# Optimization experiments

Measured on AMD Instinct MI355X. Metric: run time of the kernel, lower is better.

Reference implementation:

```python
import jax, jax.numpy as jnp
import numpy as np

B, IN, H, NOPT = 16384, 4096, 128, 64
GAIN = 0.5  # default control_gains value in the module


def gru_cell(x, h, Wih, Whh, bih, bhh):
    # torch GRU single step; gate order r, z, n
    gi = x @ Wih + bih          # [B, 3H]
    gh = h @ Whh + bhh          # [B, 3H]
    ir, iz, inn = jnp.split(gi, 3, axis=-1)
    hr, hz, hn = jnp.split(gh, 3, axis=-1)
    r = jax.nn.sigmoid(ir + hr)
    z = jax.nn.sigmoid(iz + hz)
    n = jnp.tanh(inn + r * hn)
    return (1.0 - z) * n + z * h


def setup_inputs() -> dict:
    key = jax.random.key(0)
    ks = jax.random.split(key, 12)
    s = lambda k, shape: (jax.random.normal(k, shape, jnp.float32) * 0.05)
    return {
        "obs": jax.random.normal(ks[0], (B, IN), jnp.float32),
        "chosen_option": jax.random.randint(ks[1], (B,), 0, NOPT),
        "h0": jnp.zeros((B, H), jnp.float32),
        "h1": jnp.zeros((B, H), jnp.float32),
        "Wa": s(ks[2], (IN, H)), "ba": jnp.zeros((H,), jnp.float32),
        "Wih0": s(ks[3], (H, 3 * H)), "Whh0": s(ks[4], (H, 3 * H)),
        "bih0": jnp.zeros((3 * H,), jnp.float32), "bhh0": jnp.zeros((3 * H,), jnp.float32),
        "Wih1": s(ks[5], (2 * H, 3 * H)), "Whh1": s(ks[6], (H, 3 * H)),
        "bih1": jnp.zeros((3 * H,), jnp.float32), "bhh1": jnp.zeros((3 * H,), jnp.float32),
        "Wv0": s(ks[7], (H, NOPT)), "bv0": jnp.zeros((NOPT,), jnp.float32),
        "Wv1": s(ks[8], (H, NOPT)), "bv1": jnp.zeros((NOPT,), jnp.float32),
        "Wt0": s(ks[9], (H, NOPT)), "bt0": jnp.zeros((NOPT,), jnp.float32),
    }


def reference(obs, chosen_option, h0, h1, Wa, ba, Wih0, Whh0, bih0, bhh0,
              Wih1, Whh1, bih1, bhh1, Wv0, bv0, Wv1, bv1, Wt0, bt0):
    # attention: tanh(Linear(obs))
    attn = jnp.tanh(obs @ Wa + ba)                       # [B, H]
    # layer 0: GRU on attn
    h0n = gru_cell(attn, h0, Wih0, Whh0, bih0, bhh0)     # [B, H]
    hc0 = (h0n - 0.5) * GAIN + 0.5                       # gain contrast
    v0 = hc0 @ Wv0 + bv0                                 # [B, NOPT]
    term = jax.nn.sigmoid(hc0 @ Wt0 + bt0)               # [B, NOPT]
    term_p = jnp.take_along_axis(term, chosen_option[:, None], axis=1)  # [B, 1]
    # layer 1: GRU on cat(attn, own hidden)
    x1 = jnp.concatenate([attn, h1], axis=-1)            # [B, 2H]
    h1n = gru_cell(x1, h1, Wih1, Whh1, bih1, bhh1)       # [B, H]
    hc1 = (h1n - 0.5) * GAIN + 0.5
    v1 = hc1 @ Wv1 + bv1                                 # [B, NOPT]
    return v0, term_p, v1, h0n, h1n
```

## Files before the change

kernel.cpp:

```cpp
#include <hip/hip_runtime.h>
#include <hip/hip_bf16.h>
#include <stdint.h>


typedef __attribute__((ext_vector_type(8))) short bf16x8;
typedef __attribute__((ext_vector_type(4))) float f32x4;
typedef __attribute__((ext_vector_type(8))) float f32x8;

#define INDIM 4096
#define H 128
#define NOPT 64

#define WS_WAT    0u
#define WS_WIH0T  524288u
#define WS_WHH0T  573440u
#define WS_WIH1T  622592u
#define WS_WHH1T  720896u
#define WS_WV0T   770048u
#define WS_WV1T   778240u
#define WS_WT0T   786432u
#define WS_ATTN   794624u

#define OUT_V0    0u
#define OUT_TERMP 1048576u
#define OUT_V1    1064960u
#define OUT_H0N   2113536u
#define OUT_H1N   4210688u

typedef __attribute__((address_space(1))) const void gas_t;
typedef __attribute__((address_space(3))) void las_t;
static __device__ __forceinline__ void gll16(const void* g, void* l) {
  __builtin_amdgcn_global_load_lds((gas_t*)g, (las_t*)l, 16, 0, 0);
}

static __device__ __forceinline__ uint16_t f2bf(float f) {
  __hip_bfloat16 h = __float2bfloat16(f);
  return __builtin_bit_cast(uint16_t, h);
}
static __device__ __forceinline__ float sigm(float x) { return 1.0f / (1.0f + __expf(-x)); }
static __device__ __forceinline__ float fast_tanh(float x) {
  float e = __expf(2.0f * x);
  return 1.0f - 2.0f / (e + 1.0f);
}
static __device__ __forceinline__ f32x4 mfma16(bf16x8 a, bf16x8 b, f32x4 c) {
  return __builtin_amdgcn_mfma_f32_16x16x32_bf16(a, b, c, 0, 0, 0);
}
static __device__ __forceinline__ bf16x8 cvt8(f32x8 v) {
  bf16x8 r;
#pragma unroll
  for (int j = 0; j < 8; ++j) r[j] = (short)f2bf(v[j]);
  return r;
}

__global__ void k_transpose(const float* __restrict__ Wa,
                            const float* __restrict__ Wih0,
                            const float* __restrict__ Whh0,
                            const float* __restrict__ Wih1,
                            const float* __restrict__ Whh1,
                            const float* __restrict__ Wv0,
                            const float* __restrict__ Wv1,
                            const float* __restrict__ Wt0,
                            uint16_t* __restrict__ ws) {
  __shared__ float sT[32][34];
  int blk = blockIdx.x;
  const float* in; uint16_t* out; int K; int N; int base;
  if (blk < 512)      { in = Wa;   out = ws + WS_WAT;   K = 4096; N = 128; base = 0; }
  else if (blk < 560) { in = Wih0; out = ws + WS_WIH0T; K = 128;  N = 384; base = 512; }
  else if (blk < 608) { in = Whh0; out = ws + WS_WHH0T; K = 128;  N = 384; base = 560; }
  else if (blk < 704) { in = Wih1; out = ws + WS_WIH1T; K = 256;  N = 384; base = 608; }
  else if (blk < 752) { in = Whh1; out = ws + WS_WHH1T; K = 128;  N = 384; base = 704; }
  else if (blk < 760) { in = Wv0;  out = ws + WS_WV0T;  K = 128;  N = 64;  base = 752; }
  else if (blk < 768) { in = Wv1;  out = ws + WS_WV1T;  K = 128;  N = 64;  base = 760; }
  else                { in = Wt0;  out = ws + WS_WT0T;  K = 128;  N = 64;  base = 768; }
  const int tix = blk - base;
  const int nTK = K >> 5;
  const int kt = tix & (nTK - 1);
  const int nt = tix / nTK;
  const int k0 = kt * 32, n0 = nt * 32;
  const int t = threadIdx.x;
#pragma unroll
  for (int i = 0; i < 4; ++i) {
    int e = i * 256 + t, kk = e >> 5, nn = e & 31;
    sT[kk][nn] = in[(size_t)(k0 + kk) * N + n0 + nn];
  }
  __syncthreads();
#pragma unroll
  for (int i = 0; i < 4; ++i) {
    int e = i * 256 + t, nn = e >> 5, kk = e & 31;
    out[(size_t)(n0 + nn) * K + k0 + kk] = f2bf(sT[kk][nn]);
  }
}

__launch_bounds__(256, 2)
__global__ void k_attn(const float* __restrict__ obs,
                       uint16_t* __restrict__ ws,
                       const float* __restrict__ ba) {
  __shared__ __align__(16) uint16_t sA[2][32 * 8 * 8];
  __shared__ __align__(16) uint16_t sB[2][128 * 8 * 8];
  const uint16_t* WaT = ws + WS_WAT;
  uint16_t* attn = ws + WS_ATTN;
  const int t = threadIdx.x, w = t >> 6, lane = t & 63;
  const int l15 = lane & 15, quad = lane >> 4;
  const int wm = w >> 1, wn = w & 1;
  const int row0 = blockIdx.x * 32;
  const int rA = wm * 16 + l15;
  const int sr = t >> 3, sg = t & 7;
  const float* aSrc = obs + (size_t)(row0 + sr) * INDIM + sg * 8;
  const int aDst = (sr * 8 + (sg ^ (sr & 7))) * 8;
  const int n0 = w * 32 + (lane >> 3);
  const int gsrc = (lane & 7) ^ (n0 & 7);
  const uint16_t* bSrc = WaT + (size_t)n0 * INDIM + gsrc * 8;

  f32x4 acc[4] = {};

  auto compute = [&](int buf) {
#pragma unroll
    for (int ks = 0; ks < 2; ++ks) {
      bf16x8 a = *(const bf16x8*)&sA[buf][(rA * 8 + ((ks * 4 + quad) ^ (rA & 7))) * 8];
#pragma unroll
      for (int nb = 0; nb < 4; ++nb) {
        const int n = wn * 64 + nb * 16 + l15;
        bf16x8 b = *(const bf16x8*)&sB[buf][(n * 8 + ((ks * 4 + quad) ^ (n & 7))) * 8];
        acc[nb] = mfma16(a, b, acc[nb]);
      }
    }
  };

  {
    f32x8 av = *(const f32x8*)aSrc;
#pragma unroll
    for (int j = 0; j < 4; ++j)
      gll16(bSrc + (size_t)j * 8 * INDIM, (void*)&sB[0][(w * 4 + j) * 512]);
    *(bf16x8*)&sA[0][aDst] = cvt8(av);
  }
  __syncthreads();

  for (int kt = 0; kt < 63; ++kt) {
    const int cur = kt & 1, nxt = cur ^ 1;
    f32x8 av = *(const f32x8*)(aSrc + (size_t)(kt + 1) * 64);
#pragma unroll
    for (int j = 0; j < 4; ++j)
      gll16(bSrc + (size_t)(kt + 1) * 64 + (size_t)j * 8 * INDIM,
            (void*)&sB[nxt][(w * 4 + j) * 512]);
    compute(cur);
    *(bf16x8*)&sA[nxt][aDst] = cvt8(av);
    __syncthreads();
  }
  compute(1);

#pragma unroll
  for (int nb = 0; nb < 4; ++nb) {
    const int col = wn * 64 + nb * 16 + l15;
    const float bav = ba[col];
#pragma unroll
    for (int i = 0; i < 4; ++i) {
      const int r = wm * 16 + quad * 4 + i;
      attn[(size_t)(row0 + r) * H + col] = f2bf(fast_tanh(acc[nb][i] + bav));
    }
  }
}

__launch_bounds__(256, 2)
__global__ void k_gru(const uint16_t* __restrict__ ws,
                      const float* __restrict__ h0,
                      const float* __restrict__ bih0,
                      const float* __restrict__ bhh0,
                      const float* __restrict__ bv0,
                      const float* __restrict__ bt0,
                      const int* __restrict__ chosen,
                      const float* __restrict__ h1,
                      const float* __restrict__ bih1,
                      const float* __restrict__ bhh1,
                      const float* __restrict__ bv1,
                      float* __restrict__ out) {
  __shared__ __align__(16) uint16_t sC[32 * 16 * 8];
  const uint16_t* attn  = ws + WS_ATTN;
  const uint16_t* Wih0T = ws + WS_WIH0T;
  const uint16_t* Whh0T = ws + WS_WHH0T;
  const uint16_t* Wih1T = ws + WS_WIH1T;
  const uint16_t* Whh1T = ws + WS_WHH1T;
  const uint16_t* Wv0T  = ws + WS_WV0T;
  const uint16_t* Wv1T  = ws + WS_WV1T;
  const uint16_t* Wt0T  = ws + WS_WT0T;
  const int t = threadIdx.x, w = t >> 6, lane = t & 63;
  const int l15 = lane & 15, quad = lane >> 4;
  const int wm = w >> 1, wn = w & 1;
  const int row0 = blockIdx.x * 32;
  const int rA = wm * 16 + l15;

  bf16x8 ax[4], ah[4];
#pragma unroll
  for (int ks = 0; ks < 4; ++ks) {
    ax[ks] = *(const bf16x8*)(attn + (size_t)(row0 + rA) * H + ks * 32 + quad * 8);
    ah[ks] = cvt8(*(const f32x8*)(h0 + (size_t)(row0 + rA) * H + ks * 32 + quad * 8));
  }

#pragma unroll
  for (int nbl = 0; nbl < 4; ++nbl) {
    const int nb = wn * 4 + nbl;
    const int nrow = nb * 16 + l15;
    f32x4 air = {}, ahr = {}, aiz = {}, ahz = {}, ain = {}, ahn = {};
#pragma unroll
    for (int ks = 0; ks < 4; ++ks) {
      const int k = ks * 32 + quad * 8;
      bf16x8 b0 = *(const bf16x8*)(Wih0T + (size_t)(nrow      ) * H + k);
      bf16x8 b1 = *(const bf16x8*)(Wih0T + (size_t)(nrow + 128) * H + k);
      bf16x8 b2 = *(const bf16x8*)(Wih0T + (size_t)(nrow + 256) * H + k);
      bf16x8 b3 = *(const bf16x8*)(Whh0T + (size_t)(nrow      ) * H + k);
      bf16x8 b4 = *(const bf16x8*)(Whh0T + (size_t)(nrow + 128) * H + k);
      bf16x8 b5 = *(const bf16x8*)(Whh0T + (size_t)(nrow + 256) * H + k);
      air = mfma16(ax[ks], b0, air);
      aiz = mfma16(ax[ks], b1, aiz);
      ain = mfma16(ax[ks], b2, ain);
      ahr = mfma16(ah[ks], b3, ahr);
      ahz = mfma16(ah[ks], b4, ahz);
      ahn = mfma16(ah[ks], b5, ahn);
    }
    const int col = nrow;
    const float b_ir = bih0[col],       b_hr = bhh0[col];
    const float b_iz = bih0[col + 128], b_hz = bhh0[col + 128];
    const float b_in = bih0[col + 256], b_hn = bhh0[col + 256];
    const int kb = col >> 3;
#pragma unroll
    for (int i = 0; i < 4; ++i) {
      const int r = wm * 16 + quad * 4 + i;
      const int grow = row0 + r;
      const float rr = sigm(air[i] + ahr[i] + b_ir + b_hr);
      const float zz = sigm(aiz[i] + ahz[i] + b_iz + b_hz);
      const float nn = fast_tanh(ain[i] + b_in + rr * (ahn[i] + b_hn));
      const float hv = h0[(size_t)grow * H + col];
      const float hnew = (1.0f - zz) * nn + zz * hv;
      out[OUT_H0N + (size_t)grow * H + col] = hnew;
      sC[(r * 16 + (kb ^ (r & 7))) * 8 + (col & 7)] = f2bf(0.5f * hnew + 0.25f);
    }
  }
  __syncthreads();

  {
    bf16x8 ac[4];
#pragma unroll
    for (int ks = 0; ks < 4; ++ks)
      ac[ks] = *(const bf16x8*)&sC[(rA * 16 + ((ks * 4 + quad) ^ (rA & 7))) * 8];
    int ch[4];
#pragma unroll
    for (int i = 0; i < 4; ++i) ch[i] = chosen[row0 + wm * 16 + quad * 4 + i];
#pragma unroll
    for (int hb = 0; hb < 2; ++hb) {
      const int colf = wn * 2 + hb;
      const int nrow = colf * 16 + l15;
      f32x4 av = {}, at = {};
#pragma unroll
      for (int ks = 0; ks < 4; ++ks) {
        const int k = ks * 32 + quad * 8;
        bf16x8 b0 = *(const bf16x8*)(Wv0T + (size_t)nrow * H + k);
        bf16x8 b1 = *(const bf16x8*)(Wt0T + (size_t)nrow * H + k);
        av = mfma16(ac[ks], b0, av);
        at = mfma16(ac[ks], b1, at);
      }
      const int col = nrow;
      const float bvv = bv0[col], btv = bt0[col];
#pragma unroll
      for (int i = 0; i < 4; ++i) {
        const int grow = row0 + wm * 16 + quad * 4 + i;
        out[OUT_V0 + (size_t)grow * NOPT + col] = av[i] + bvv;
        if (ch[i] == col)
          out[OUT_TERMP + grow] = sigm(at[i] + btv);
      }
    }
  }
  __syncthreads();

  bf16x8 ah1[4];
#pragma unroll
  for (int ks = 0; ks < 4; ++ks)
    ah1[ks] = cvt8(*(const f32x8*)(h1 + (size_t)(row0 + rA) * H + ks * 32 + quad * 8));
#pragma unroll
  for (int nbl = 0; nbl < 4; ++nbl) {
    const int nb = wn * 4 + nbl;
    const int nrow = nb * 16 + l15;
    f32x4 air = {}, ahr = {}, aiz = {}, ahz = {}, ain = {}, ahn = {};
#pragma unroll
    for (int ks = 0; ks < 8; ++ks) {
      const int k = ks * 32 + quad * 8;
      const bf16x8 a = (ks < 4) ? ax[ks] : ah1[ks - 4];
      bf16x8 b0 = *(const bf16x8*)(Wih1T + (size_t)(nrow      ) * 256 + k);
      bf16x8 b1 = *(const bf16x8*)(Wih1T + (size_t)(nrow + 128) * 256 + k);
      bf16x8 b2 = *(const bf16x8*)(Wih1T + (size_t)(nrow + 256) * 256 + k);
      air = mfma16(a, b0, air);
      aiz = mfma16(a, b1, aiz);
      ain = mfma16(a, b2, ain);
    }
#pragma unroll
    for (int ks = 0; ks < 4; ++ks) {
      const int k = ks * 32 + quad * 8;
      bf16x8 b0 = *(const bf16x8*)(Whh1T + (size_t)(nrow      ) * H + k);
      bf16x8 b1 = *(const bf16x8*)(Whh1T + (size_t)(nrow + 128) * H + k);
      bf16x8 b2 = *(const bf16x8*)(Whh1T + (size_t)(nrow + 256) * H + k);
      ahr = mfma16(ah1[ks], b0, ahr);
      ahz = mfma16(ah1[ks], b1, ahz);
      ahn = mfma16(ah1[ks], b2, ahn);
    }
    const int col = nrow;
    const float b_ir = bih1[col],       b_hr = bhh1[col];
    const float b_iz = bih1[col + 128], b_hz = bhh1[col + 128];
    const float b_in = bih1[col + 256], b_hn = bhh1[col + 256];
    const int kb = col >> 3;
#pragma unroll
    for (int i = 0; i < 4; ++i) {
      const int r = wm * 16 + quad * 4 + i;
      const int grow = row0 + r;
      const float rr = sigm(air[i] + ahr[i] + b_ir + b_hr);
      const float zz = sigm(aiz[i] + ahz[i] + b_iz + b_hz);
      const float nn = fast_tanh(ain[i] + b_in + rr * (ahn[i] + b_hn));
      const float hv = h1[(size_t)grow * H + col];
      const float hnew = (1.0f - zz) * nn + zz * hv;
      out[OUT_H1N + (size_t)grow * H + col] = hnew;
      sC[(r * 16 + (kb ^ (r & 7))) * 8 + (col & 7)] = f2bf(0.5f * hnew + 0.25f);
    }
  }
  __syncthreads();

  {
    bf16x8 ac[4];
#pragma unroll
    for (int ks = 0; ks < 4; ++ks)
      ac[ks] = *(const bf16x8*)&sC[(rA * 16 + ((ks * 4 + quad) ^ (rA & 7))) * 8];
#pragma unroll
    for (int hb = 0; hb < 2; ++hb) {
      const int colf = wn * 2 + hb;
      const int nrow = colf * 16 + l15;
      f32x4 av = {};
#pragma unroll
      for (int ks = 0; ks < 4; ++ks) {
        const int k = ks * 32 + quad * 8;
        bf16x8 b = *(const bf16x8*)(Wv1T + (size_t)nrow * H + k);
        av = mfma16(ac[ks], b, av);
      }
      const int col = nrow;
      const float bvv = bv1[col];
#pragma unroll
      for (int i = 0; i < 4; ++i) {
        const int grow = row0 + wm * 16 + quad * 4 + i;
        out[OUT_V1 + (size_t)grow * NOPT + col] = av[i] + bvv;
      }
    }
  }
}

extern "C" void kernel_launch(void* const* d_in, const int* in_sizes, int n_in,
                              void* d_out, int out_size, void* d_ws, size_t ws_size,
                              hipStream_t stream) {
  (void)in_sizes; (void)n_in; (void)out_size; (void)ws_size;
  const float* obs    = (const float*)d_in[0];
  const int*   chosen = (const int*)d_in[1];
  const float* h0     = (const float*)d_in[2];
  const float* h1     = (const float*)d_in[3];
  const float* Wa     = (const float*)d_in[4];
  const float* ba     = (const float*)d_in[5];
  const float* Wih0   = (const float*)d_in[6];
  const float* Whh0   = (const float*)d_in[7];
  const float* bih0   = (const float*)d_in[8];
  const float* bhh0   = (const float*)d_in[9];
  const float* Wih1   = (const float*)d_in[10];
  const float* Whh1   = (const float*)d_in[11];
  const float* bih1   = (const float*)d_in[12];
  const float* bhh1   = (const float*)d_in[13];
  const float* Wv0    = (const float*)d_in[14];
  const float* bv0    = (const float*)d_in[15];
  const float* Wv1    = (const float*)d_in[16];
  const float* bv1    = (const float*)d_in[17];
  const float* Wt0    = (const float*)d_in[18];
  const float* bt0    = (const float*)d_in[19];
  uint16_t* ws  = (uint16_t*)d_ws;
  float*    out = (float*)d_out;

  hipLaunchKernelGGL(k_transpose, dim3(776), dim3(256), 0, stream,
                     Wa, Wih0, Whh0, Wih1, Whh1, Wv0, Wv1, Wt0, ws);
  hipLaunchKernelGGL(k_attn, dim3(512), dim3(256), 0, stream, obs, ws, ba);
  hipLaunchKernelGGL(k_gru, dim3(512), dim3(256), 0, stream,
                     ws, h0, bih0, bhh0, bv0, bt0, chosen,
                     h1, bih1, bhh1, bv1, out);
}
```

Baseline: 499.5 us.

## Load obs directly into registers and deepen attn pipeline to four stages

The attention GEMM kernel no longer stages the fp32 obs tile through LDS. Each lane loads its MFMA A-operand fragments straight into registers and converts them to bf16 just before use. The Wa tile buffer grows from two to four LDS stages. Explicit vmcnt waits plus raw barriers keep two tiles of loads in flight while computing. This is meant to hide global-memory latency on the bandwidth-bound obs stream and remove LDS writes and reads for A, at the cost of more LDS per block (64KB), more live registers, and possible occupancy pressure.

```diff
diff --git a/kernel.cpp b/kernel.cpp
--- a/kernel.cpp
+++ b/kernel.cpp
@@ -49,6 +49,14 @@
   bf16x8 r;
 #pragma unroll
   for (int j = 0; j < 8; ++j) r[j] = (short)f2bf(v[j]);
+  return r;
+}
+static __device__ __forceinline__ bf16x8 cvt8p(f32x4 lo, f32x4 hi) {
+  bf16x8 r;
+  r[0] = (short)f2bf(lo[0]); r[1] = (short)f2bf(lo[1]);
+  r[2] = (short)f2bf(lo[2]); r[3] = (short)f2bf(lo[3]);
+  r[4] = (short)f2bf(hi[0]); r[5] = (short)f2bf(hi[1]);
+  r[6] = (short)f2bf(hi[2]); r[7] = (short)f2bf(hi[3]);
   return r;
 }
 
@@ -95,58 +103,70 @@
 __global__ void k_attn(const float* __restrict__ obs,
                        uint16_t* __restrict__ ws,
                        const float* __restrict__ ba) {
-  __shared__ __align__(16) uint16_t sA[2][32 * 8 * 8];
-  __shared__ __align__(16) uint16_t sB[2][128 * 8 * 8];
+  __shared__ __align__(16) uint16_t sB[4][128 * 64];
   const uint16_t* WaT = ws + WS_WAT;
   uint16_t* attn = ws + WS_ATTN;
   const int t = threadIdx.x, w = t >> 6, lane = t & 63;
   const int l15 = lane & 15, quad = lane >> 4;
   const int wm = w >> 1, wn = w & 1;
   const int row0 = blockIdx.x * 32;
-  const int rA = wm * 16 + l15;
-  const int sr = t >> 3, sg = t & 7;
-  const float* aSrc = obs + (size_t)(row0 + sr) * INDIM + sg * 8;
-  const int aDst = (sr * 8 + (sg ^ (sr & 7))) * 8;
+  const float* aPtr = obs + (size_t)(row0 + wm * 16 + l15) * INDIM + quad * 8;
   const int n0 = w * 32 + (lane >> 3);
   const int gsrc = (lane & 7) ^ (n0 & 7);
   const uint16_t* bSrc = WaT + (size_t)n0 * INDIM + gsrc * 8;
 
   f32x4 acc[4] = {};
-
-  auto compute = [&](int buf) {
-#pragma unroll
-    for (int ks = 0; ks < 2; ++ks) {
-      bf16x8 a = *(const bf16x8*)&sA[buf][(rA * 8 + ((ks * 4 + quad) ^ (rA & 7))) * 8];
-#pragma unroll
-      for (int nb = 0; nb < 4; ++nb) {
-        const int n = wn * 64 + nb * 16 + l15;
-        bf16x8 b = *(const bf16x8*)&sB[buf][(n * 8 + ((ks * 4 + quad) ^ (n & 7))) * 8];
-        acc[nb] = mfma16(a, b, acc[nb]);
-      }
-    }
-  };
-
-  {
-    f32x8 av = *(const f32x8*)aSrc;
-#pragma unroll
-    for (int j = 0; j < 4; ++j)
-      gll16(bSrc + (size_t)j * 8 * INDIM, (void*)&sB[0][(w * 4 + j) * 512]);
-    *(bf16x8*)&sA[0][aDst] = cvt8(av);
-  }
-  __syncthreads();
-
-  for (int kt = 0; kt < 63; ++kt) {
-    const int cur = kt & 1, nxt = cur ^ 1;
-    f32x8 av = *(const f32x8*)(aSrc + (size_t)(kt + 1) * 64);
-#pragma unroll
-    for (int j = 0; j < 4; ++j)
-      gll16(bSrc + (size_t)(kt + 1) * 64 + (size_t)j * 8 * INDIM,
-            (void*)&sB[nxt][(w * 4 + j) * 512]);
-    compute(cur);
-    *(bf16x8*)&sA[nxt][aDst] = cvt8(av);
-    __syncthreads();
-  }
-  compute(1);
+  f32x4 A0[4], A1[4], A2[4], A3[4];
+
+#define ISSUE_A(S, tt) do {                                     \
+    S[0] = *(const f32x4*)(aPtr + (size_t)(tt) * 64);           \
+    S[1] = *(const f32x4*)(aPtr + (size_t)(tt) * 64 + 4);       \
+    S[2] = *(const f32x4*)(aPtr + (size_t)(tt) * 64 + 32);      \
+    S[3] = *(const f32x4*)(aPtr + (size_t)(tt) * 64 + 36);      \
+  } while (0)
+#define ISSUE_B(bufj, tt) do {                                              \
+    _Pragma("unroll")                                                       \
+    for (int j = 0; j < 4; ++j)                                             \
+      gll16(bSrc + (size_t)(tt) * 64 + (size_t)j * 8 * INDIM,               \
+            (void*)&sB[bufj][(w * 4 + j) * 512]);                           \
+  } while (0)
+#define COMPUTE(S, bufj) do {                                               \
+    _Pragma("unroll")                                                       \
+    for (int ks = 0; ks < 2; ++ks) {                                        \
+      bf16x8 a = cvt8p(S[ks * 2], S[ks * 2 + 1]);                           \
+      _Pragma("unroll")                                                     \
+      for (int nb = 0; nb < 4; ++nb) {                                      \
+        const int n = wn * 64 + nb * 16 + l15;                              \
+        bf16x8 b = *(const bf16x8*)                                         \
+            &sB[bufj][(n * 8 + ((ks * 4 + quad) ^ (n & 7))) * 8];           \
+        acc[nb] = mfma16(a, b, acc[nb]);                                    \
+      }                                                                     \
+    }                                                                       \
+  } while (0)
+#define BARN(N) do {                                                        \
+    asm volatile("s_waitcnt vmcnt(" #N ")" ::: "memory");                   \
+    __builtin_amdgcn_sched_barrier(0);                                      \
+    __builtin_amdgcn_s_barrier();                                           \
+    __builtin_amdgcn_sched_barrier(0);                                      \
+  } while (0)
+
+  ISSUE_A(A0, 0); ISSUE_B(0, 0);
+  ISSUE_A(A1, 1); ISSUE_B(1, 1);
+  BARN(8);
+  for (int kt4 = 0; kt4 < 60; kt4 += 4) {
+    ISSUE_A(A2, kt4 + 2); ISSUE_B(2, kt4 + 2); COMPUTE(A0, 0); BARN(8);
+    ISSUE_A(A3, kt4 + 3); ISSUE_B(3, kt4 + 3); COMPUTE(A1, 1); BARN(8);
+    ISSUE_A(A0, kt4 + 4); ISSUE_B(0, kt4 + 4); COMPUTE(A2, 2); BARN(8);
+    ISSUE_A(A1, kt4 + 5); ISSUE_B(1, kt4 + 5); COMPUTE(A3, 3); BARN(8);
+  }
+  ISSUE_A(A2, 62); ISSUE_B(2, 62); COMPUTE(A0, 0); BARN(8);
+  ISSUE_A(A3, 63); ISSUE_B(3, 63); COMPUTE(A1, 1); BARN(8);
+  COMPUTE(A2, 2); BARN(0);
+  COMPUTE(A3, 3);
+#undef ISSUE_A
+#undef ISSUE_B
+#undef COMPUTE
+#undef BARN
 
 #pragma unroll
   for (int nb = 0; nb < 4; ++nb) {
```

Measured after the change: 499.0 us. No clear change (-0.1%).
